# Kernel tuning notes

Hardware: AMD Instinct MI355X
Metric: run time of the kernel (lower is better)

Reference implementation:

```python
import jax, jax.numpy as jnp
import numpy as np

B, S, H, I, E, TOP_K = 2, 1024, 1024, 2048, 8, 2


def setup_inputs() -> dict:
    key = jax.random.key(0)
    ks = jax.random.split(key, 5)
    return {
        "hidden_states": jax.random.normal(ks[0], (B, S, H), jnp.float32),
        # torch Linear weights are (out, in)
        "router_w": jax.random.normal(ks[1], (E, H), jnp.float32) * 0.02,
        "w1": jax.random.normal(ks[2], (E, I, H), jnp.float32) * 0.02,
        "v": jax.random.normal(ks[3], (E, I, H), jnp.float32) * 0.02,
        "w2": jax.random.normal(ks[4], (E, H, I), jnp.float32) * 0.02,
    }


def _moe(x, router_w, w1, v, w2):
    # x: [T, H] flattened tokens
    T = x.shape[0]
    n_exp = router_w.shape[0]
    logits = x @ router_w.T                                    # [T, E]
    probs = jax.nn.softmax(logits.astype(jnp.float32), axis=-1)
    top_p, top_i = jax.lax.top_k(probs, TOP_K)                 # [T, K]
    top_p = top_p / top_p.sum(axis=-1, keepdims=True)
    top_p = top_p.astype(x.dtype)
    # dense gate matrix [T, E]; zero for unselected experts -> identical math
    # to the torch gather / index_add combine
    gates = jnp.zeros((T, n_exp), x.dtype).at[
        jnp.arange(T)[:, None], top_i].set(top_p)
    out = jnp.zeros_like(x)
    for e in range(n_exp):  # small fixed expert loop keeps peak memory low
        h = jax.nn.gelu(x @ w1[e].T, approximate=False) * (x @ v[e].T)  # [T, I]
        out = out + gates[:, e:e + 1] * (h @ w2[e].T)                   # [T, H]
    return out, logits


def reference(hidden_states, router_w, w1, v, w2):
    b, s, h = hidden_states.shape
    out, logits = _moe(hidden_states.reshape(-1, h), router_w, w1, v, w2)
    return out.reshape(b, s, h), logits
```

## Files before the change

kernel.cpp:

```cpp
#include <hip/hip_runtime.h>
#include <math.h>

#define T 2048
#define HD 1024
#define ID 2048
#define NE 8

typedef short bf16x8 __attribute__((ext_vector_type(8)));
typedef float f32x4 __attribute__((ext_vector_type(4)));
typedef unsigned short u16x8 __attribute__((ext_vector_type(8)));

__device__ __forceinline__ unsigned short f2bf(float f) {
  union { float f; unsigned u; } v; v.f = f;
  unsigned r = v.u + 0x7FFFu + ((v.u >> 16) & 1u);
  return (unsigned short)(r >> 16);
}

__device__ __forceinline__ u16x8 cvt8(float4 a, float4 b) {
  u16x8 o;
  o[0] = f2bf(a.x); o[1] = f2bf(a.y); o[2] = f2bf(a.z); o[3] = f2bf(a.w);
  o[4] = f2bf(b.x); o[5] = f2bf(b.y); o[6] = f2bf(b.z); o[7] = f2bf(b.w);
  return o;
}

__device__ __forceinline__ void glds16(const unsigned short* g, unsigned short* l) {
  __builtin_amdgcn_global_load_lds(
      (const __attribute__((address_space(1))) unsigned int*)(g),
      (__attribute__((address_space(3))) unsigned int*)(l), 16, 0, 0);
}

__global__ __launch_bounds__(256) void cast_x_kernel(
    const float* __restrict__ x, unsigned short* __restrict__ xb) {
  size_t idx = ((size_t)blockIdx.x * 256 + threadIdx.x) * 8;
  float4 f0 = *(const float4*)(x + idx);
  float4 f1 = *(const float4*)(x + idx + 4);
  *(u16x8*)(xb + idx) = cvt8(f0, f1);
}

__global__ __launch_bounds__(256) void cast_w_kernel(
    const float* __restrict__ s0, const float* __restrict__ s1,
    const float* __restrict__ s2, unsigned short* __restrict__ d0,
    unsigned short* __restrict__ d1, unsigned short* __restrict__ d2) {
  const float* s; unsigned short* d;
  if (blockIdx.y == 0)      { s = s0; d = d0; }
  else if (blockIdx.y == 1) { s = s1; d = d1; }
  else                      { s = s2; d = d2; }
  size_t idx = ((size_t)blockIdx.x * 256 + threadIdx.x) * 8;
  float4 f0 = *(const float4*)(s + idx);
  float4 f1 = *(const float4*)(s + idx + 4);
  *(u16x8*)(d + idx) = cvt8(f0, f1);
}

__global__ __launch_bounds__(256) void router_kernel(
    const float* __restrict__ x, const float* __restrict__ rw,
    float* __restrict__ logits_out, int* __restrict__ pair_rowid,
    float* __restrict__ pair_gate, int* __restrict__ counts) {
  __shared__ float rws[NE * HD];
  int tid = threadIdx.x;
  for (int j = tid * 4; j < NE * HD; j += 256 * 4)
    *(float4*)&rws[j] = *(const float4*)&rw[j];
  __syncthreads();
  int wid = tid >> 6, lane = tid & 63;
  int t = blockIdx.x * 4 + wid;
  float acc[NE];
#pragma unroll
  for (int e = 0; e < NE; e++) acc[e] = 0.f;
  const float* xrow = x + (size_t)t * HD;
  for (int j = 0; j < HD; j += 64) {
    float xv = xrow[j + lane];
#pragma unroll
    for (int e = 0; e < NE; e++) acc[e] += xv * rws[e * HD + j + lane];
  }
#pragma unroll
  for (int e = 0; e < NE; e++)
    for (int off = 32; off > 0; off >>= 1) acc[e] += __shfl_xor(acc[e], off, 64);
  if (lane == 0) {
#pragma unroll
    for (int e = 0; e < NE; e++) logits_out[t * NE + e] = acc[e];
    int e0 = 0;
#pragma unroll
    for (int e = 1; e < NE; e++) if (acc[e] > acc[e0]) e0 = e;
    int e1 = (e0 == 0) ? 1 : 0;
#pragma unroll
    for (int e = 0; e < NE; e++)
      if (e != e0 && e != e1 && acc[e] > acc[e1]) e1 = e;
    float b = __expf(acc[e1] - acc[e0]);
    float g0 = 1.f / (1.f + b);
    float g1 = 1.f - g0;
    int p0 = atomicAdd(&counts[e0], 1);
    pair_rowid[e0 * T + p0] = t * 2;
    pair_gate[e0 * T + p0] = g0;
    int p1 = atomicAdd(&counts[e1], 1);
    pair_rowid[e1 * T + p1] = t * 2 + 1;
    pair_gate[e1 * T + p1] = g1;
  }
}

__global__ __launch_bounds__(256) void gemm1_kernel(
    const unsigned short* __restrict__ xb, const unsigned short* __restrict__ w1b,
    const unsigned short* __restrict__ vb, unsigned short* __restrict__ hb,
    const int* __restrict__ pair_rowid, const int* __restrict__ counts) {
  int e = blockIdx.z;
  int cnt = counts[e];
  int row0 = blockIdx.y * 128;
  if (row0 >= cnt) return;
  __shared__ unsigned short As[128 * 64];
  __shared__ unsigned short B1s[64 * 64];
  __shared__ unsigned short B2s[64 * 64];
  __shared__ int rids[128];
  int tid = threadIdx.x;
  if (tid < 128) {
    int idx = row0 + tid; if (idx > cnt - 1) idx = cnt - 1;
    rids[tid] = pair_rowid[e * T + idx];
  }
  __syncthreads();
  int lane = tid & 63, wid = tid >> 6;
  int wr = wid >> 1, wc = wid & 1;
  int col0 = blockIdx.x * 64;
  int gr = lane >> 3, gc = lane & 7;
  const unsigned short *aA[4], *aB1[2], *aB2[2];
#pragma unroll
  for (int c = 0; c < 4; c++) {
    int row = (c * 4 + wid) * 8 + gr;
    int tok = rids[row] >> 1;
    aA[c] = xb + (size_t)tok * HD + ((gc ^ (row & 7)) * 8);
  }
#pragma unroll
  for (int c = 0; c < 2; c++) {
    int row = (c * 4 + wid) * 8 + gr;
    int kswz = ((gc ^ (row & 7)) * 8);
    aB1[c] = w1b + ((size_t)(e * ID + col0 + row)) * HD + kswz;
    aB2[c] = vb  + ((size_t)(e * ID + col0 + row)) * HD + kswz;
  }
  f32x4 acc1[4][2] = {};
  f32x4 acc3[4][2] = {};
  int mrow = lane & 15, kq = lane >> 4;
  int swzm = mrow & 7;
  for (int kt = 0; kt < HD; kt += 64) {
#pragma unroll
    for (int c = 0; c < 4; c++)
      glds16(aA[c] + kt, &As[(c * 4 + wid) * 512]);
#pragma unroll
    for (int c = 0; c < 2; c++) {
      glds16(aB1[c] + kt, &B1s[(c * 4 + wid) * 512]);
      glds16(aB2[c] + kt, &B2s[(c * 4 + wid) * 512]);
    }
    __syncthreads();
#pragma unroll
    for (int kk = 0; kk < 2; kk++) {
      int g = kk * 4 + kq;
      int ko = ((g ^ swzm) * 8);
      bf16x8 a[4], b1[2], b2[2];
#pragma unroll
      for (int mi = 0; mi < 4; mi++)
        a[mi] = *(const bf16x8*)&As[(wr * 64 + mi * 16 + mrow) * 64 + ko];
#pragma unroll
      for (int ni = 0; ni < 2; ni++) {
        b1[ni] = *(const bf16x8*)&B1s[(wc * 32 + ni * 16 + mrow) * 64 + ko];
        b2[ni] = *(const bf16x8*)&B2s[(wc * 32 + ni * 16 + mrow) * 64 + ko];
      }
#pragma unroll
      for (int mi = 0; mi < 4; mi++)
#pragma unroll
        for (int ni = 0; ni < 2; ni++) {
          acc1[mi][ni] = __builtin_amdgcn_mfma_f32_16x16x32_bf16(a[mi], b1[ni], acc1[mi][ni], 0, 0, 0);
          acc3[mi][ni] = __builtin_amdgcn_mfma_f32_16x16x32_bf16(a[mi], b2[ni], acc3[mi][ni], 0, 0, 0);
        }
    }
    __syncthreads();
  }
  int dcol = lane & 15, drow4 = (lane >> 4) * 4;
#pragma unroll
  for (int mi = 0; mi < 4; mi++)
#pragma unroll
    for (int ni = 0; ni < 2; ni++)
#pragma unroll
      for (int r = 0; r < 4; r++) {
        int lr = wr * 64 + mi * 16 + drow4 + r;
        if (row0 + lr < cnt) {
          float g1v = acc1[mi][ni][r];
          float g3v = acc3[mi][ni][r];
          float hval = 0.5f * g1v * (1.f + erff(g1v * 0.70710678118654752f)) * g3v;
          int rowid = rids[lr];
          hb[(size_t)rowid * ID + col0 + wc * 32 + ni * 16 + dcol] = f2bf(hval);
        }
      }
}

__global__ __launch_bounds__(256) void gemm2_kernel(
    const unsigned short* __restrict__ hb, const unsigned short* __restrict__ w2b,
    float* __restrict__ out, const int* __restrict__ pair_rowid,
    const float* __restrict__ pair_gate, const int* __restrict__ counts) {
  int e = blockIdx.z;
  int cnt = counts[e];
  int row0 = blockIdx.y * 64;
  if (row0 >= cnt) return;
  __shared__ unsigned short As[64 * 64];
  __shared__ unsigned short Bs[64 * 64];
  __shared__ int rids[64];
  __shared__ float gts[64];
  int tid = threadIdx.x;
  if (tid < 64) {
    int idx = row0 + tid; if (idx > cnt - 1) idx = cnt - 1;
    rids[tid] = pair_rowid[e * T + idx];
    gts[tid] = pair_gate[e * T + idx];
  }
  __syncthreads();
  int lane = tid & 63, wid = tid >> 6;
  int wr = wid >> 1, wc = wid & 1;
  int col0 = blockIdx.x * 64;
  int gr = lane >> 3, gc = lane & 7;
  const unsigned short *aA[2], *aB[2];
#pragma unroll
  for (int c = 0; c < 2; c++) {
    int row = (c * 4 + wid) * 8 + gr;
    int kswz = ((gc ^ (row & 7)) * 8);
    aA[c] = hb  + (size_t)rids[row] * ID + kswz;
    aB[c] = w2b + ((size_t)(e * HD + col0 + row)) * ID + kswz;
  }
  f32x4 acc[2][2] = {};
  int mrow = lane & 15, kq = lane >> 4;
  int swzm = mrow & 7;
  for (int kt = 0; kt < ID; kt += 64) {
#pragma unroll
    for (int c = 0; c < 2; c++) {
      glds16(aA[c] + kt, &As[(c * 4 + wid) * 512]);
      glds16(aB[c] + kt, &Bs[(c * 4 + wid) * 512]);
    }
    __syncthreads();
#pragma unroll
    for (int kk = 0; kk < 2; kk++) {
      int g = kk * 4 + kq;
      int ko = ((g ^ swzm) * 8);
      bf16x8 a[2], b[2];
#pragma unroll
      for (int mi = 0; mi < 2; mi++)
        a[mi] = *(const bf16x8*)&As[(wr * 32 + mi * 16 + mrow) * 64 + ko];
#pragma unroll
      for (int ni = 0; ni < 2; ni++)
        b[ni] = *(const bf16x8*)&Bs[(wc * 32 + ni * 16 + mrow) * 64 + ko];
#pragma unroll
      for (int mi = 0; mi < 2; mi++)
#pragma unroll
        for (int ni = 0; ni < 2; ni++)
          acc[mi][ni] = __builtin_amdgcn_mfma_f32_16x16x32_bf16(a[mi], b[ni], acc[mi][ni], 0, 0, 0);
    }
    __syncthreads();
  }
  int dcol = lane & 15, drow4 = (lane >> 4) * 4;
#pragma unroll
  for (int mi = 0; mi < 2; mi++)
#pragma unroll
    for (int ni = 0; ni < 2; ni++)
#pragma unroll
      for (int r = 0; r < 4; r++) {
        int lr = wr * 32 + mi * 16 + drow4 + r;
        if (row0 + lr < cnt) {
          int tokrow = rids[lr] >> 1;
          float val = gts[lr] * acc[mi][ni][r];
          atomicAdd(&out[(size_t)tokrow * HD + col0 + wc * 32 + ni * 16 + dcol], val);
        }
      }
}

extern "C" void kernel_launch(void* const* d_in, const int* in_sizes, int n_in,
                              void* d_out, int out_size, void* d_ws, size_t ws_size,
                              hipStream_t stream) {
  const float* x  = (const float*)d_in[0];
  const float* rw = (const float*)d_in[1];
  const float* w1 = (const float*)d_in[2];
  const float* v  = (const float*)d_in[3];
  const float* w2 = (const float*)d_in[4];
  float* out = (float*)d_out;
  float* logits_out = out + (size_t)T * HD;

  char* ws = (char*)d_ws;
  unsigned short* xb  = (unsigned short*)(ws);
  unsigned short* hb  = (unsigned short*)(ws + (4u << 20));
  unsigned short* w1b = (unsigned short*)(ws + (20u << 20));
  unsigned short* vb  = (unsigned short*)(ws + (52u << 20));
  unsigned short* w2b = (unsigned short*)(ws + (84u << 20));
  int*   pair_rowid   = (int*)  (ws + (116u << 20));
  float* pair_gate    = (float*)(ws + (116u << 20) + 65536);
  int*   counts       = (int*)  (ws + (116u << 20) + 131072);

  hipMemsetAsync(out, 0, (size_t)T * HD * sizeof(float), stream);
  hipMemsetAsync(counts, 0, NE * sizeof(int), stream);

  cast_w_kernel<<<dim3(8192, 3), 256, 0, stream>>>(w1, v, w2, w1b, vb, w2b);
  cast_x_kernel<<<(T * HD) / (256 * 8), 256, 0, stream>>>(x, xb);
  router_kernel<<<T / 4, 256, 0, stream>>>(x, rw, logits_out, pair_rowid,
                                           pair_gate, counts);
  gemm1_kernel<<<dim3(ID / 64, T / 128, NE), 256, 0, stream>>>(
      xb, w1b, vb, hb, pair_rowid, counts);
  gemm2_kernel<<<dim3(HD / 64, T / 64, NE), 256, 0, stream>>>(
      hb, w2b, out, pair_rowid, pair_gate, counts);
}
```

Baseline: 394.1 us.

## Fuse weight/x casts with router and overlap w2 cast with gemm1

Merges the x cast, w1/v casts and router into a single prep kernel with block ranges dispatched by block index, and has each thread convert 16 elements. The w2 cast is moved into extra blocks of the gemm1 grid so its memory traffic can overlap with gemm1 compute. This removes separate kernel launches and their serialization, at the cost of blocks with different resource needs sharing a launch (router shared memory is sized for every block) and possible contention with gemm1.

```diff
diff --git a/kernel.cpp b/kernel.cpp
--- a/kernel.cpp
+++ b/kernel.cpp
@@ -23,45 +23,50 @@
   return o;
 }
 
+__device__ __forceinline__ void cast_chunk16(const float* __restrict__ s,
+                                             unsigned short* __restrict__ d,
+                                             size_t base) {
+  size_t idx = base + (size_t)threadIdx.x * 16;
+  float4 f0 = *(const float4*)(s + idx);
+  float4 f1 = *(const float4*)(s + idx + 4);
+  float4 f2 = *(const float4*)(s + idx + 8);
+  float4 f3 = *(const float4*)(s + idx + 12);
+  *(u16x8*)(d + idx) = cvt8(f0, f1);
+  *(u16x8*)(d + idx + 8) = cvt8(f2, f3);
+}
+
 __device__ __forceinline__ void glds16(const unsigned short* g, unsigned short* l) {
   __builtin_amdgcn_global_load_lds(
       (const __attribute__((address_space(1))) unsigned int*)(g),
       (__attribute__((address_space(3))) unsigned int*)(l), 16, 0, 0);
 }
 
-__global__ __launch_bounds__(256) void cast_x_kernel(
-    const float* __restrict__ x, unsigned short* __restrict__ xb) {
-  size_t idx = ((size_t)blockIdx.x * 256 + threadIdx.x) * 8;
-  float4 f0 = *(const float4*)(x + idx);
-  float4 f1 = *(const float4*)(x + idx + 4);
-  *(u16x8*)(xb + idx) = cvt8(f0, f1);
-}
-
-__global__ __launch_bounds__(256) void cast_w_kernel(
-    const float* __restrict__ s0, const float* __restrict__ s1,
-    const float* __restrict__ s2, unsigned short* __restrict__ d0,
-    unsigned short* __restrict__ d1, unsigned short* __restrict__ d2) {
-  const float* s; unsigned short* d;
-  if (blockIdx.y == 0)      { s = s0; d = d0; }
-  else if (blockIdx.y == 1) { s = s1; d = d1; }
-  else                      { s = s2; d = d2; }
-  size_t idx = ((size_t)blockIdx.x * 256 + threadIdx.x) * 8;
-  float4 f0 = *(const float4*)(s + idx);
-  float4 f1 = *(const float4*)(s + idx + 4);
-  *(u16x8*)(d + idx) = cvt8(f0, f1);
-}
-
-__global__ __launch_bounds__(256) void router_kernel(
+__global__ __launch_bounds__(256) void prep_kernel(
     const float* __restrict__ x, const float* __restrict__ rw,
-    float* __restrict__ logits_out, int* __restrict__ pair_rowid,
-    float* __restrict__ pair_gate, int* __restrict__ counts) {
+    const float* __restrict__ w1, const float* __restrict__ v,
+    unsigned short* __restrict__ xb, unsigned short* __restrict__ w1b,
+    unsigned short* __restrict__ vb, float* __restrict__ logits_out,
+    int* __restrict__ pair_rowid, float* __restrict__ pair_gate,
+    int* __restrict__ counts) {
+  int bx = blockIdx.x;
+  if (bx >= 1024) {
+    int cid = bx - 1024;
+    const float* s = (cid < 4096) ? w1 : v;
+    unsigned short* d = (cid < 4096) ? w1b : vb;
+    cast_chunk16(s, d, (size_t)(cid & 4095) * 4096);
+    return;
+  }
+  if (bx >= 512) {
+    cast_chunk16(x, xb, (size_t)(bx - 512) * 4096);
+    return;
+  }
   __shared__ float rws[NE * HD];
   int tid = threadIdx.x;
   for (int j = tid * 4; j < NE * HD; j += 256 * 4)
     *(float4*)&rws[j] = *(const float4*)&rw[j];
   __syncthreads();
   int wid = tid >> 6, lane = tid & 63;
-  int t = blockIdx.x * 4 + wid;
+  int t = bx * 4 + wid;
   float acc[NE];
 #pragma unroll
   for (int e = 0; e < NE; e++) acc[e] = 0.f;
@@ -99,7 +104,13 @@
 __global__ __launch_bounds__(256) void gemm1_kernel(
     const unsigned short* __restrict__ xb, const unsigned short* __restrict__ w1b,
     const unsigned short* __restrict__ vb, unsigned short* __restrict__ hb,
+    const float* __restrict__ w2, unsigned short* __restrict__ w2b,
     const int* __restrict__ pair_rowid, const int* __restrict__ counts) {
+  if (blockIdx.x >= 32) {
+    int cid = (blockIdx.x - 32) + 32 * (blockIdx.y + 16 * blockIdx.z);
+    cast_chunk16(w2, w2b, (size_t)cid * 4096);
+    return;
+  }
   int e = blockIdx.z;
   int cnt = counts[e];
   int row0 = blockIdx.y * 128;
@@ -287,12 +298,11 @@
   hipMemsetAsync(out, 0, (size_t)T * HD * sizeof(float), stream);
   hipMemsetAsync(counts, 0, NE * sizeof(int), stream);
 
-  cast_w_kernel<<<dim3(8192, 3), 256, 0, stream>>>(w1, v, w2, w1b, vb, w2b);
-  cast_x_kernel<<<(T * HD) / (256 * 8), 256, 0, stream>>>(x, xb);
-  router_kernel<<<T / 4, 256, 0, stream>>>(x, rw, logits_out, pair_rowid,
-                                           pair_gate, counts);
-  gemm1_kernel<<<dim3(ID / 64, T / 128, NE), 256, 0, stream>>>(
-      xb, w1b, vb, hb, pair_rowid, counts);
+  prep_kernel<<<9216, 256, 0, stream>>>(x, rw, w1, v, xb, w1b, vb,
+                                        logits_out, pair_rowid, pair_gate,
+                                        counts);
+  gemm1_kernel<<<dim3(ID / 64 + 32, T / 128, NE), 256, 0, stream>>>(
+      xb, w1b, vb, hb, w2, w2b, pair_rowid, counts);
   gemm2_kernel<<<dim3(HD / 64, T / 64, NE), 256, 0, stream>>>(
       hb, w2b, out, pair_rowid, pair_gate, counts);
 }
```

After: 367.5 us. 1.07x faster.
